# Kernel optimization log

Hardware: AMD Instinct MI355X
Metric: run time of the kernel (lower is better)

Reference implementation:

```python
import jax, jax.numpy as jnp
import numpy as np

B, S, D = 4, 2048, 512
H, DK, DV = 8, 64, 64
LN_EPS = 1e-5


def setup_inputs() -> dict:
    key = jax.random.key(0)
    ks = jax.random.split(key, 9)
    inp = {
        "input_Q": jax.random.normal(ks[0], (B, S, D), jnp.float32),
        "input_K": jax.random.normal(ks[1], (B, S, D), jnp.float32),
        "input_V": jax.random.normal(ks[2], (B, S, D), jnp.float32),
        "attn_mask": jax.random.bernoulli(ks[3], 0.1, (B, S, S)),
        # weights stored [in, out] (math-equivalent to torch Linear's x @ W.T)
        "W_Q": jax.random.normal(ks[4], (D, H * DK), jnp.float32) * (1.0 / np.sqrt(D)),
        "W_K": jax.random.normal(ks[5], (D, H * DK), jnp.float32) * (1.0 / np.sqrt(D)),
        "W_V": jax.random.normal(ks[6], (D, H * DV), jnp.float32) * (1.0 / np.sqrt(D)),
        "W_fc": jax.random.normal(ks[7], (H * DV, D), jnp.float32) * (1.0 / np.sqrt(H * DV)),
        "ln_gamma": jnp.ones((D,), jnp.float32),
        "ln_beta": jnp.zeros((D,), jnp.float32),
    }
    return inp


def _mha(input_Q, input_K, input_V, attn_mask, W_Q, W_K, W_V, W_fc, ln_gamma, ln_beta):
    # project and split heads -> [B, H, S, d]
    Q = (input_Q @ W_Q).reshape(B, S, H, DK).transpose(0, 2, 1, 3)
    K = (input_K @ W_K).reshape(B, S, H, DK).transpose(0, 2, 1, 3)
    V = (input_V @ W_V).reshape(B, S, H, DV).transpose(0, 2, 1, 3)
    # scaled dot-product attention with masking (mask broadcast over heads)
    scores = jnp.einsum('bhqd,bhkd->bhqk', Q, K) / np.sqrt(DK)
    scores = jnp.where(attn_mask[:, None, :, :], -1e9, scores)
    attn = jax.nn.softmax(scores, axis=-1)
    context = jnp.einsum('bhqk,bhkd->bhqd', attn, V)
    context = context.transpose(0, 2, 1, 3).reshape(B, S, H * DV)
    out = context @ W_fc + input_Q  # fc + residual
    # LayerNorm over last dim
    mu = jnp.mean(out, axis=-1, keepdims=True)
    var = jnp.var(out, axis=-1, keepdims=True)
    normed = (out - mu) * jax.lax.rsqrt(var + LN_EPS) * ln_gamma + ln_beta
    return normed, attn


def reference(input_Q, input_K, input_V, attn_mask, W_Q, W_K, W_V, W_fc, ln_gamma, ln_beta):
    return _mha(input_Q, input_K, input_V, attn_mask, W_Q, W_K, W_V, W_fc, ln_gamma, ln_beta)
```

## Files before the change

kernel.cpp:

```cpp
#include <hip/hip_runtime.h>
#include <stdint.h>

typedef __attribute__((ext_vector_type(8))) short short8;
typedef __attribute__((ext_vector_type(4))) float f32x4;
typedef __attribute__((ext_vector_type(4))) unsigned short ushort4v;

__device__ __forceinline__ unsigned short f2bf(float f) {
    union { float f; uint32_t u; } v; v.f = f;
    return (unsigned short)((v.u + 0x7FFFu + ((v.u >> 16) & 1u)) >> 16);
}
__device__ __forceinline__ float bf2f(unsigned short h) {
    union { uint32_t u; float f; } v; v.u = ((uint32_t)h) << 16;
    return v.f;
}

__global__ __launch_bounds__(256) void prep_wt_kernel(
    const float* __restrict__ W0, const float* __restrict__ W1,
    const float* __restrict__ W2, const float* __restrict__ W3,
    unsigned short* __restrict__ Wt)
{
    const float* W = blockIdx.y == 0 ? W0 : blockIdx.y == 1 ? W1 : blockIdx.y == 2 ? W2 : W3;
    unsigned short* dst = Wt + (size_t)blockIdx.y * (512 * 512);
    int k = blockIdx.x >> 1;
    int n = ((blockIdx.x & 1) << 8) + threadIdx.x;
    dst[(size_t)n * 512 + k] = f2bf(W[(size_t)k * 512 + n]);
}

__global__ __launch_bounds__(512) void proj_kernel(
    const float* __restrict__ inQ, const float* __restrict__ inK, const float* __restrict__ inV,
    const unsigned short* __restrict__ Wt,
    unsigned short* __restrict__ outQ, unsigned short* __restrict__ outK,
    unsigned short* __restrict__ outVT)
{
    const int which = blockIdx.y;
    const float* inp = which == 0 ? inQ : which == 1 ? inK : inV;
    const unsigned short* Wtb = Wt + (size_t)which * (512 * 512);
    const int tid = threadIdx.x;
    const int wid = tid >> 6, l = tid & 63;
    const int rt = wid >> 1, ch = wid & 1;
    const int lrow = l & 15, g = l >> 4;
    const int rowbase = blockIdx.x * 64;
    const int arow = rowbase + rt * 16 + lrow;

    f32x4 acc[16];
#pragma unroll
    for (int t = 0; t < 16; ++t) acc[t] = (f32x4){0.f, 0.f, 0.f, 0.f};

    for (int k0 = 0; k0 < 512; k0 += 32) {
        const float* ap = inp + (size_t)arow * 512 + k0 + g * 8;
        float4 a0 = *(const float4*)ap;
        float4 a1 = *(const float4*)(ap + 4);
        short8 af;
        af[0] = (short)f2bf(a0.x); af[1] = (short)f2bf(a0.y);
        af[2] = (short)f2bf(a0.z); af[3] = (short)f2bf(a0.w);
        af[4] = (short)f2bf(a1.x); af[5] = (short)f2bf(a1.y);
        af[6] = (short)f2bf(a1.z); af[7] = (short)f2bf(a1.w);
#pragma unroll
        for (int t = 0; t < 16; ++t) {
            const int n = ch * 256 + t * 16 + lrow;
            short8 bf = *(const short8*)(Wtb + (size_t)n * 512 + k0 + g * 8);
            acc[t] = __builtin_amdgcn_mfma_f32_16x16x32_bf16(af, bf, acc[t], 0, 0, 0);
        }
    }

    if (which == 2) {
#pragma unroll
        for (int t = 0; t < 16; ++t) {
            const int n = ch * 256 + t * 16 + lrow;
            const int hh = n >> 6, dd = n & 63;
            const int row0 = rowbase + rt * 16 + g * 4;
            const int bb = row0 >> 11, s0 = row0 & 2047;
            ushort4v pk;
            pk[0] = f2bf(acc[t][0]); pk[1] = f2bf(acc[t][1]);
            pk[2] = f2bf(acc[t][2]); pk[3] = f2bf(acc[t][3]);
            *(ushort4v*)(outVT + ((size_t)(bb * 8 + hh) * 64 + dd) * 2048 + s0) = pk;
        }
    } else {
        unsigned short* dst = which == 0 ? outQ : outK;
#pragma unroll
        for (int t = 0; t < 16; ++t) {
            const int n = ch * 256 + t * 16 + lrow;
            const int hh = n >> 6, dd = n & 63;
#pragma unroll
            for (int r = 0; r < 4; ++r) {
                const int row = rowbase + rt * 16 + g * 4 + r;
                const int bb = row >> 11, s0 = row & 2047;
                dst[((size_t)(bb * 8 + hh) * 2048 + s0) * 64 + dd] = f2bf(acc[t][r]);
            }
        }
    }
}

__global__ __launch_bounds__(512) void attn_kernel(
    const unsigned short* __restrict__ Qw, const unsigned short* __restrict__ Kw,
    const unsigned short* __restrict__ VT, const unsigned char* __restrict__ mask,
    float* __restrict__ attn_out, unsigned short* __restrict__ ctx)
{
    extern __shared__ char smem[];
    float* rowsum = (float*)(smem + 128 * 1024);
    const int L = blockIdx.x;
    const int xcd = L & 7, idx = L >> 3;
    const int q6 = idx & 63;
    const int bh = ((idx >> 6) << 3) | xcd;
    const int b = bh >> 3, h = bh & 7;
    const int qg0 = q6 * 32;
    const int tid = threadIdx.x, wid = tid >> 6, l = tid & 63;
    const int lrow = l & 15, g = l >> 4;

    if (tid < 32) rowsum[tid] = 0.f;
    __syncthreads();

    {
        const int qt = wid & 1, stripe = wid >> 1;
        const int q0 = qt * 16;
        const unsigned short* qp = Qw + ((size_t)bh * 2048 + qg0 + q0 + lrow) * 64 + g * 8;
        const short8 qf0 = *(const short8*)qp;
        const short8 qf1 = *(const short8*)(qp + 32);
        float psum[4] = {0.f, 0.f, 0.f, 0.f};
        const size_t mbase = ((size_t)b * 2048 + qg0 + q0 + g * 4) * 2048;
        for (int i = 0; i < 32; ++i) {
            const int kbase = (stripe + i * 4) * 16;
            const unsigned short* kp = Kw + ((size_t)bh * 2048 + kbase + lrow) * 64 + g * 8;
            short8 kf0 = *(const short8*)kp;
            short8 kf1 = *(const short8*)(kp + 32);
            f32x4 sc = (f32x4){0.f, 0.f, 0.f, 0.f};
            sc = __builtin_amdgcn_mfma_f32_16x16x32_bf16(qf0, kf0, sc, 0, 0, 0);
            sc = __builtin_amdgcn_mfma_f32_16x16x32_bf16(qf1, kf1, sc, 0, 0, 0);
#pragma unroll
            for (int r = 0; r < 4; ++r) {
                const int qrl = q0 + g * 4 + r;
                const unsigned char m = mask[mbase + (size_t)r * 2048 + kbase + lrow];
                const float e = m ? 0.f : __expf(sc[r] * 0.125f);
                psum[r] += e;
                *(unsigned short*)(smem + qrl * 4096 +
                                   (((kbase + lrow) * 2) ^ ((qrl & 7) << 4))) = f2bf(e);
            }
        }
#pragma unroll
        for (int r = 0; r < 4; ++r) {
            psum[r] += __shfl_xor(psum[r], 1);
            psum[r] += __shfl_xor(psum[r], 2);
            psum[r] += __shfl_xor(psum[r], 4);
            psum[r] += __shfl_xor(psum[r], 8);
        }
        if (lrow == 0) {
#pragma unroll
            for (int r = 0; r < 4; ++r) atomicAdd(&rowsum[q0 + g * 4 + r], psum[r]);
        }
    }
    __syncthreads();

    if (wid < 4) {
        const int ct = wid;
        f32x4 accA = (f32x4){0.f,0.f,0.f,0.f}, accB = (f32x4){0.f,0.f,0.f,0.f};
        const unsigned short* vbase = VT + ((size_t)bh * 64 + ct * 16 + lrow) * 2048;
        const int rA = lrow, rB = 16 + lrow;
        const int swA = (rA & 7) << 4, swB = (rB & 7) << 4;
#pragma unroll 4
        for (int ks = 0; ks < 64; ++ks) {
            short8 bf = *(const short8*)(vbase + ks * 32 + g * 8);
            const int kbyte = ks * 64 + g * 16;
            short8 a0 = *(const short8*)(smem + rA * 4096 + (kbyte ^ swA));
            short8 a1 = *(const short8*)(smem + rB * 4096 + (kbyte ^ swB));
            accA = __builtin_amdgcn_mfma_f32_16x16x32_bf16(a0, bf, accA, 0, 0, 0);
            accB = __builtin_amdgcn_mfma_f32_16x16x32_bf16(a1, bf, accB, 0, 0, 0);
        }
#pragma unroll
        for (int rt = 0; rt < 2; ++rt) {
            const f32x4 a = rt ? accB : accA;
#pragma unroll
            for (int r = 0; r < 4; ++r) {
                const int row = rt * 16 + g * 4 + r;
                const float rinv = 1.0f / rowsum[row];
                ctx[((size_t)b * 2048 + qg0 + row) * 512 + h * 64 + ct * 16 + lrow] =
                    f2bf(a[r] * rinv);
            }
        }
    } else {
        const int r0 = (wid - 4) * 8;
        for (int rr = 0; rr < 8; ++rr) {
            const int row = r0 + rr;
            const float rinv = 1.0f / rowsum[row];
            float* gp = attn_out + ((size_t)bh * 2048 + qg0 + row) * 2048;
            const int sw = (row & 7) << 4;
            const int rbase = row * 4096;
#pragma unroll 4
            for (int c0 = 0; c0 < 2048; c0 += 128) {
                const int off = rbase + (((c0 + 2 * l) * 2) ^ sw);
                const uint32_t u = *(const uint32_t*)(smem + off);
                float2 o;
                o.x = bf2f((unsigned short)(u & 0xFFFFu)) * rinv;
                o.y = bf2f((unsigned short)(u >> 16)) * rinv;
                *(float2*)(gp + c0 + 2 * l) = o;
            }
        }
    }
}

__global__ __launch_bounds__(512) void fc_ln_kernel(
    const unsigned short* __restrict__ ctx, const unsigned short* __restrict__ Wtfc,
    const float* __restrict__ resid, const float* __restrict__ gamma,
    const float* __restrict__ beta, float* __restrict__ out)
{
    __shared__ float red[64][2][2];
    const int tid = threadIdx.x;
    const int wid = tid >> 6, l = tid & 63;
    const int rt = wid >> 1, ch = wid & 1;
    const int lrow = l & 15, g = l >> 4;
    const int rowbase = blockIdx.x * 64;
    const int arow = rowbase + rt * 16 + lrow;

    f32x4 acc[16];
#pragma unroll
    for (int t = 0; t < 16; ++t) acc[t] = (f32x4){0.f, 0.f, 0.f, 0.f};

    for (int k0 = 0; k0 < 512; k0 += 32) {
        short8 af = *(const short8*)(ctx + (size_t)arow * 512 + k0 + g * 8);
#pragma unroll
        for (int t = 0; t < 16; ++t) {
            const int n = ch * 256 + t * 16 + lrow;
            short8 bf = *(const short8*)(Wtfc + (size_t)n * 512 + k0 + g * 8);
            acc[t] = __builtin_amdgcn_mfma_f32_16x16x32_bf16(af, bf, acc[t], 0, 0, 0);
        }
    }

    float s1[4] = {0,0,0,0}, s2[4] = {0,0,0,0};
#pragma unroll
    for (int t = 0; t < 16; ++t) {
        const int n = ch * 256 + t * 16 + lrow;
#pragma unroll
        for (int r = 0; r < 4; ++r) {
            const int row = rowbase + rt * 16 + g * 4 + r;
            float v = acc[t][r] + resid[(size_t)row * 512 + n];
            acc[t][r] = v;
            s1[r] += v;
            s2[r] += v * v;
        }
    }
#pragma unroll
    for (int r = 0; r < 4; ++r) {
        s1[r] += __shfl_xor(s1[r], 1); s2[r] += __shfl_xor(s2[r], 1);
        s1[r] += __shfl_xor(s1[r], 2); s2[r] += __shfl_xor(s2[r], 2);
        s1[r] += __shfl_xor(s1[r], 4); s2[r] += __shfl_xor(s2[r], 4);
        s1[r] += __shfl_xor(s1[r], 8); s2[r] += __shfl_xor(s2[r], 8);
    }
    if (lrow == 0) {
#pragma unroll
        for (int r = 0; r < 4; ++r) {
            red[rt * 16 + g * 4 + r][ch][0] = s1[r];
            red[rt * 16 + g * 4 + r][ch][1] = s2[r];
        }
    }
    __syncthreads();
    float mean[4], rstd[4];
#pragma unroll
    for (int r = 0; r < 4; ++r) {
        const int rl = rt * 16 + g * 4 + r;
        const float S1 = red[rl][0][0] + red[rl][1][0];
        const float S2 = red[rl][0][1] + red[rl][1][1];
        mean[r] = S1 * (1.0f / 512.0f);
        const float var = S2 * (1.0f / 512.0f) - mean[r] * mean[r];
        rstd[r] = rsqrtf(var + 1e-5f);
    }
#pragma unroll
    for (int t = 0; t < 16; ++t) {
        const int n = ch * 256 + t * 16 + lrow;
        const float gm = gamma[n], bt = beta[n];
#pragma unroll
        for (int r = 0; r < 4; ++r) {
            const int row = rowbase + rt * 16 + g * 4 + r;
            out[(size_t)row * 512 + n] = (acc[t][r] - mean[r]) * rstd[r] * gm + bt;
        }
    }
}

extern "C" void kernel_launch(void* const* d_in, const int* in_sizes, int n_in,
                              void* d_out, int out_size, void* d_ws, size_t ws_size,
                              hipStream_t stream)
{
    (void)in_sizes; (void)n_in; (void)out_size; (void)ws_size;
    const float* inQ = (const float*)d_in[0];
    const float* inK = (const float*)d_in[1];
    const float* inV = (const float*)d_in[2];
    const unsigned char* mask = (const unsigned char*)d_in[3];
    const float* WQ  = (const float*)d_in[4];
    const float* WK  = (const float*)d_in[5];
    const float* WV  = (const float*)d_in[6];
    const float* Wfc = (const float*)d_in[7];
    const float* gamma = (const float*)d_in[8];
    const float* beta  = (const float*)d_in[9];

    char* ws = (char*)d_ws;
    unsigned short* wsQ   = (unsigned short*)(ws);
    unsigned short* wsK   = (unsigned short*)(ws + ((size_t)8  << 20));
    unsigned short* wsVT  = (unsigned short*)(ws + ((size_t)16 << 20));
    unsigned short* wsCtx = (unsigned short*)(ws + ((size_t)24 << 20));
    unsigned short* wsWt  = (unsigned short*)(ws + ((size_t)32 << 20));

    float* out_ln   = (float*)d_out;
    float* out_attn = out_ln + (size_t)4 * 2048 * 512;

    prep_wt_kernel<<<dim3(1024, 4), dim3(256), 0, stream>>>(WQ, WK, WV, Wfc, wsWt);
    proj_kernel<<<dim3(128, 3), dim3(512), 0, stream>>>(inQ, inK, inV, wsWt, wsQ, wsK, wsVT);

    const int smem_bytes = 128 * 1024 + 128;
    hipFuncSetAttribute((const void*)attn_kernel,
                        hipFuncAttributeMaxDynamicSharedMemorySize, smem_bytes);
    attn_kernel<<<dim3(2048), dim3(512), smem_bytes, stream>>>(wsQ, wsK, wsVT, mask,
                                                               out_attn, wsCtx);
    fc_ln_kernel<<<dim3(128), dim3(512), 0, stream>>>(wsCtx, wsWt + (size_t)3 * 512 * 512,
                                                      inQ, gamma, beta, out_ln);
}
```

Measured before the change: 1.046 ms.

## Shrink attention tiles, tile weight transpose, split-bf16 projections, fp32 context

```diff
diff --git a/kernel.cpp b/kernel.cpp
--- a/kernel.cpp
+++ b/kernel.cpp
@@ -19,14 +19,27 @@
     const float* __restrict__ W2, const float* __restrict__ W3,
     unsigned short* __restrict__ Wt)
 {
+    __shared__ unsigned short tile[64][66];
     const float* W = blockIdx.y == 0 ? W0 : blockIdx.y == 1 ? W1 : blockIdx.y == 2 ? W2 : W3;
     unsigned short* dst = Wt + (size_t)blockIdx.y * (512 * 512);
-    int k = blockIdx.x >> 1;
-    int n = ((blockIdx.x & 1) << 8) + threadIdx.x;
-    dst[(size_t)n * 512 + k] = f2bf(W[(size_t)k * 512 + n]);
-}
-
-__global__ __launch_bounds__(512) void proj_kernel(
+    const int k0 = (blockIdx.x >> 3) * 64;
+    const int n0 = (blockIdx.x & 7) * 64;
+    const int nx = threadIdx.x & 63;
+    const int ty = threadIdx.x >> 6;
+#pragma unroll
+    for (int i = 0; i < 16; ++i) {
+        const int kl = i * 4 + ty;
+        tile[nx][kl] = f2bf(W[(size_t)(k0 + kl) * 512 + n0 + nx]);
+    }
+    __syncthreads();
+#pragma unroll
+    for (int i = 0; i < 16; ++i) {
+        const int nl = i * 4 + ty;
+        dst[(size_t)(n0 + nl) * 512 + k0 + nx] = tile[nl][nx];
+    }
+}
+
+__global__ __launch_bounds__(256) void proj_kernel(
     const float* __restrict__ inQ, const float* __restrict__ inK, const float* __restrict__ inV,
     const unsigned short* __restrict__ Wt,
     unsigned short* __restrict__ outQ, unsigned short* __restrict__ outK,
@@ -39,7 +52,7 @@
     const int wid = tid >> 6, l = tid & 63;
     const int rt = wid >> 1, ch = wid & 1;
     const int lrow = l & 15, g = l >> 4;
-    const int rowbase = blockIdx.x * 64;
+    const int rowbase = blockIdx.x * 32;
     const int arow = rowbase + rt * 16 + lrow;
 
     f32x4 acc[16];
@@ -50,16 +63,20 @@
         const float* ap = inp + (size_t)arow * 512 + k0 + g * 8;
         float4 a0 = *(const float4*)ap;
         float4 a1 = *(const float4*)(ap + 4);
-        short8 af;
-        af[0] = (short)f2bf(a0.x); af[1] = (short)f2bf(a0.y);
-        af[2] = (short)f2bf(a0.z); af[3] = (short)f2bf(a0.w);
-        af[4] = (short)f2bf(a1.x); af[5] = (short)f2bf(a1.y);
-        af[6] = (short)f2bf(a1.z); af[7] = (short)f2bf(a1.w);
+        float av[8] = {a0.x, a0.y, a0.z, a0.w, a1.x, a1.y, a1.z, a1.w};
+        short8 hi, lo;
+#pragma unroll
+        for (int j = 0; j < 8; ++j) {
+            unsigned short hb = f2bf(av[j]);
+            hi[j] = (short)hb;
+            lo[j] = (short)f2bf(av[j] - bf2f(hb));
+        }
 #pragma unroll
         for (int t = 0; t < 16; ++t) {
             const int n = ch * 256 + t * 16 + lrow;
             short8 bf = *(const short8*)(Wtb + (size_t)n * 512 + k0 + g * 8);
-            acc[t] = __builtin_amdgcn_mfma_f32_16x16x32_bf16(af, bf, acc[t], 0, 0, 0);
+            acc[t] = __builtin_amdgcn_mfma_f32_16x16x32_bf16(hi, bf, acc[t], 0, 0, 0);
+            acc[t] = __builtin_amdgcn_mfma_f32_16x16x32_bf16(lo, bf, acc[t], 0, 0, 0);
         }
     }
 
@@ -91,123 +108,113 @@
     }
 }
 
-__global__ __launch_bounds__(512) void attn_kernel(
+__global__ __launch_bounds__(256) void attn_kernel(
     const unsigned short* __restrict__ Qw, const unsigned short* __restrict__ Kw,
     const unsigned short* __restrict__ VT, const unsigned char* __restrict__ mask,
-    float* __restrict__ attn_out, unsigned short* __restrict__ ctx)
+    float* __restrict__ attn_out, float* __restrict__ ctx)
 {
     extern __shared__ char smem[];
-    float* rowsum = (float*)(smem + 128 * 1024);
+    float* rowsum = (float*)(smem + 16 * 4096);
     const int L = blockIdx.x;
     const int xcd = L & 7, idx = L >> 3;
-    const int q6 = idx & 63;
-    const int bh = ((idx >> 6) << 3) | xcd;
+    const int q7 = idx & 127;
+    const int bh = ((idx >> 7) << 3) | xcd;
     const int b = bh >> 3, h = bh & 7;
-    const int qg0 = q6 * 32;
+    const int qg0 = q7 * 16;
     const int tid = threadIdx.x, wid = tid >> 6, l = tid & 63;
     const int lrow = l & 15, g = l >> 4;
 
-    if (tid < 32) rowsum[tid] = 0.f;
+    if (tid < 16) rowsum[tid] = 0.f;
     __syncthreads();
 
     {
-        const int qt = wid & 1, stripe = wid >> 1;
-        const int q0 = qt * 16;
-        const unsigned short* qp = Qw + ((size_t)bh * 2048 + qg0 + q0 + lrow) * 64 + g * 8;
+        const unsigned short* qp = Qw + ((size_t)bh * 2048 + qg0 + lrow) * 64 + g * 8;
         const short8 qf0 = *(const short8*)qp;
         const short8 qf1 = *(const short8*)(qp + 32);
-        float psum[4] = {0.f, 0.f, 0.f, 0.f};
-        const size_t mbase = ((size_t)b * 2048 + qg0 + q0 + g * 4) * 2048;
+        float psum = 0.f;
+        const unsigned char* mrow = mask + ((size_t)b * 2048 + qg0 + lrow) * 2048;
+        const int sw = (lrow & 7) << 4;
+        char* prow = smem + lrow * 4096;
+#pragma unroll 2
         for (int i = 0; i < 32; ++i) {
-            const int kbase = (stripe + i * 4) * 16;
+            const int kbase = (wid + i * 4) * 16;
             const unsigned short* kp = Kw + ((size_t)bh * 2048 + kbase + lrow) * 64 + g * 8;
             short8 kf0 = *(const short8*)kp;
             short8 kf1 = *(const short8*)(kp + 32);
             f32x4 sc = (f32x4){0.f, 0.f, 0.f, 0.f};
-            sc = __builtin_amdgcn_mfma_f32_16x16x32_bf16(qf0, kf0, sc, 0, 0, 0);
-            sc = __builtin_amdgcn_mfma_f32_16x16x32_bf16(qf1, kf1, sc, 0, 0, 0);
+            sc = __builtin_amdgcn_mfma_f32_16x16x32_bf16(kf0, qf0, sc, 0, 0, 0);
+            sc = __builtin_amdgcn_mfma_f32_16x16x32_bf16(kf1, qf1, sc, 0, 0, 0);
+            const uint32_t m4 = *(const uint32_t*)(mrow + kbase + g * 4);
+            ushort4v pk;
 #pragma unroll
             for (int r = 0; r < 4; ++r) {
-                const int qrl = q0 + g * 4 + r;
-                const unsigned char m = mask[mbase + (size_t)r * 2048 + kbase + lrow];
-                const float e = m ? 0.f : __expf(sc[r] * 0.125f);
-                psum[r] += e;
-                *(unsigned short*)(smem + qrl * 4096 +
-                                   (((kbase + lrow) * 2) ^ ((qrl & 7) << 4))) = f2bf(e);
+                const float e = ((m4 >> (8 * r)) & 255u) ? 0.f
+                                : exp2f(sc[r] * 0.180336880f);
+                psum += e;
+                pk[r] = f2bf(e);
             }
+            *(ushort4v*)(prow + ((kbase * 2 + g * 8) ^ sw)) = pk;
+        }
+        psum += __shfl_xor(psum, 16);
+        psum += __shfl_xor(psum, 32);
+        if (l < 16) atomicAdd(&rowsum[l], psum);
+    }
+    __syncthreads();
+
+    {
+        const int ct = wid;
+        f32x4 acc0 = (f32x4){0.f,0.f,0.f,0.f}, acc1 = (f32x4){0.f,0.f,0.f,0.f};
+        const unsigned short* vb = VT + ((size_t)bh * 64 + ct * 16 + lrow) * 2048 + g * 8;
+        char* prow = smem + lrow * 4096;
+        const int sw = (lrow & 7) << 4;
+        for (int ks = 0; ks < 64; ks += 2) {
+            short8 pa0 = *(const short8*)(prow + ((ks * 64 + g * 16) ^ sw));
+            short8 vb0 = *(const short8*)(vb + ks * 32);
+            acc0 = __builtin_amdgcn_mfma_f32_16x16x32_bf16(pa0, vb0, acc0, 0, 0, 0);
+            short8 pa1 = *(const short8*)(prow + (((ks + 1) * 64 + g * 16) ^ sw));
+            short8 vb1 = *(const short8*)(vb + (ks + 1) * 32);
+            acc1 = __builtin_amdgcn_mfma_f32_16x16x32_bf16(pa1, vb1, acc1, 0, 0, 0);
         }
 #pragma unroll
         for (int r = 0; r < 4; ++r) {
-            psum[r] += __shfl_xor(psum[r], 1);
-            psum[r] += __shfl_xor(psum[r], 2);
-            psum[r] += __shfl_xor(psum[r], 4);
-            psum[r] += __shfl_xor(psum[r], 8);
-        }
-        if (lrow == 0) {
-#pragma unroll
-            for (int r = 0; r < 4; ++r) atomicAdd(&rowsum[q0 + g * 4 + r], psum[r]);
-        }
-    }
-    __syncthreads();
-
-    if (wid < 4) {
-        const int ct = wid;
-        f32x4 accA = (f32x4){0.f,0.f,0.f,0.f}, accB = (f32x4){0.f,0.f,0.f,0.f};
-        const unsigned short* vbase = VT + ((size_t)bh * 64 + ct * 16 + lrow) * 2048;
-        const int rA = lrow, rB = 16 + lrow;
-        const int swA = (rA & 7) << 4, swB = (rB & 7) << 4;
-#pragma unroll 4
-        for (int ks = 0; ks < 64; ++ks) {
-            short8 bf = *(const short8*)(vbase + ks * 32 + g * 8);
-            const int kbyte = ks * 64 + g * 16;
-            short8 a0 = *(const short8*)(smem + rA * 4096 + (kbyte ^ swA));
-            short8 a1 = *(const short8*)(smem + rB * 4096 + (kbyte ^ swB));
-            accA = __builtin_amdgcn_mfma_f32_16x16x32_bf16(a0, bf, accA, 0, 0, 0);
-            accB = __builtin_amdgcn_mfma_f32_16x16x32_bf16(a1, bf, accB, 0, 0, 0);
-        }
-#pragma unroll
-        for (int rt = 0; rt < 2; ++rt) {
-            const f32x4 a = rt ? accB : accA;
-#pragma unroll
-            for (int r = 0; r < 4; ++r) {
-                const int row = rt * 16 + g * 4 + r;
-                const float rinv = 1.0f / rowsum[row];
-                ctx[((size_t)b * 2048 + qg0 + row) * 512 + h * 64 + ct * 16 + lrow] =
-                    f2bf(a[r] * rinv);
-            }
-        }
-    } else {
-        const int r0 = (wid - 4) * 8;
-        for (int rr = 0; rr < 8; ++rr) {
-            const int row = r0 + rr;
+            const int q = g * 4 + r;
+            const float rinv = 1.0f / rowsum[q];
+            ctx[((size_t)b * 2048 + qg0 + q) * 512 + h * 64 + ct * 16 + lrow] =
+                (acc0[r] + acc1[r]) * rinv;
+        }
+    }
+
+    {
+#pragma unroll
+        for (int rr = 0; rr < 4; ++rr) {
+            const int row = wid * 4 + rr;
             const float rinv = 1.0f / rowsum[row];
-            float* gp = attn_out + ((size_t)bh * 2048 + qg0 + row) * 2048;
-            const int sw = (row & 7) << 4;
-            const int rbase = row * 4096;
+            float* gp = attn_out + ((size_t)bh * 2048 + qg0 + row) * 2048 + 2 * l;
+            const char* pr = smem + row * 4096;
+            const int swr = (row & 7) << 4;
 #pragma unroll 4
             for (int c0 = 0; c0 < 2048; c0 += 128) {
-                const int off = rbase + (((c0 + 2 * l) * 2) ^ sw);
-                const uint32_t u = *(const uint32_t*)(smem + off);
+                const uint32_t u = *(const uint32_t*)(pr + (((c0 + 2 * l) * 2) ^ swr));
                 float2 o;
                 o.x = bf2f((unsigned short)(u & 0xFFFFu)) * rinv;
                 o.y = bf2f((unsigned short)(u >> 16)) * rinv;
-                *(float2*)(gp + c0 + 2 * l) = o;
+                *(float2*)(gp + c0) = o;
             }
         }
     }
 }
 
-__global__ __launch_bounds__(512) void fc_ln_kernel(
-    const unsigned short* __restrict__ ctx, const unsigned short* __restrict__ Wtfc,
+__global__ __launch_bounds__(256) void fc_ln_kernel(
+    const float* __restrict__ ctx, const unsigned short* __restrict__ Wtfc,
     const float* __restrict__ resid, const float* __restrict__ gamma,
     const float* __restrict__ beta, float* __restrict__ out)
 {
-    __shared__ float red[64][2][2];
+    __shared__ float red[32][2][2];
     const int tid = threadIdx.x;
     const int wid = tid >> 6, l = tid & 63;
     const int rt = wid >> 1, ch = wid & 1;
     const int lrow = l & 15, g = l >> 4;
-    const int rowbase = blockIdx.x * 64;
+    const int rowbase = blockIdx.x * 32;
     const int arow = rowbase + rt * 16 + lrow;
 
     f32x4 acc[16];
@@ -215,12 +222,23 @@
     for (int t = 0; t < 16; ++t) acc[t] = (f32x4){0.f, 0.f, 0.f, 0.f};
 
     for (int k0 = 0; k0 < 512; k0 += 32) {
-        short8 af = *(const short8*)(ctx + (size_t)arow * 512 + k0 + g * 8);
+        const float* ap = ctx + (size_t)arow * 512 + k0 + g * 8;
+        float4 a0 = *(const float4*)ap;
+        float4 a1 = *(const float4*)(ap + 4);
+        float av[8] = {a0.x, a0.y, a0.z, a0.w, a1.x, a1.y, a1.z, a1.w};
+        short8 hi, lo;
+#pragma unroll
+        for (int j = 0; j < 8; ++j) {
+            unsigned short hb = f2bf(av[j]);
+            hi[j] = (short)hb;
+            lo[j] = (short)f2bf(av[j] - bf2f(hb));
+        }
 #pragma unroll
         for (int t = 0; t < 16; ++t) {
             const int n = ch * 256 + t * 16 + lrow;
             short8 bf = *(const short8*)(Wtfc + (size_t)n * 512 + k0 + g * 8);
-            acc[t] = __builtin_amdgcn_mfma_f32_16x16x32_bf16(af, bf, acc[t], 0, 0, 0);
+            acc[t] = __builtin_amdgcn_mfma_f32_16x16x32_bf16(hi, bf, acc[t], 0, 0, 0);
+            acc[t] = __builtin_amdgcn_mfma_f32_16x16x32_bf16(lo, bf, acc[t], 0, 0, 0);
         }
     }
 
@@ -294,20 +312,20 @@
     unsigned short* wsQ   = (unsigned short*)(ws);
     unsigned short* wsK   = (unsigned short*)(ws + ((size_t)8  << 20));
     unsigned short* wsVT  = (unsigned short*)(ws + ((size_t)16 << 20));
-    unsigned short* wsCtx = (unsigned short*)(ws + ((size_t)24 << 20));
-    unsigned short* wsWt  = (unsigned short*)(ws + ((size_t)32 << 20));
+    float*          wsCtx = (float*)         (ws + ((size_t)24 << 20));
+    unsigned short* wsWt  = (unsigned short*)(ws + ((size_t)40 << 20));
 
     float* out_ln   = (float*)d_out;
     float* out_attn = out_ln + (size_t)4 * 2048 * 512;
 
-    prep_wt_kernel<<<dim3(1024, 4), dim3(256), 0, stream>>>(WQ, WK, WV, Wfc, wsWt);
-    proj_kernel<<<dim3(128, 3), dim3(512), 0, stream>>>(inQ, inK, inV, wsWt, wsQ, wsK, wsVT);
-
-    const int smem_bytes = 128 * 1024 + 128;
+    prep_wt_kernel<<<dim3(64, 4), dim3(256), 0, stream>>>(WQ, WK, WV, Wfc, wsWt);
+    proj_kernel<<<dim3(256, 3), dim3(256), 0, stream>>>(inQ, inK, inV, wsWt, wsQ, wsK, wsVT);
+
+    const int smem_bytes = 16 * 4096 + 64;
     hipFuncSetAttribute((const void*)attn_kernel,
                         hipFuncAttributeMaxDynamicSharedMemorySize, smem_bytes);
-    attn_kernel<<<dim3(2048), dim3(512), smem_bytes, stream>>>(wsQ, wsK, wsVT, mask,
+    attn_kernel<<<dim3(4096), dim3(256), smem_bytes, stream>>>(wsQ, wsK, wsVT, mask,
                                                                out_attn, wsCtx);
-    fc_ln_kernel<<<dim3(128), dim3(512), 0, stream>>>(wsCtx, wsWt + (size_t)3 * 512 * 512,
+    fc_ln_kernel<<<dim3(256), dim3(256), 0, stream>>>(wsCtx, wsWt + (size_t)3 * 512 * 512,
                                                       inQ, gamma, beta, out_ln);
 }
```

After: 1.102 ms. +5.4%, slower.
